# Kernel tuning notes

Measured on AMD Instinct MI355X. Metric: run time of the kernel, lower is better.

The kernel has to match this reference:

```python
import jax, jax.numpy as jnp
import numpy as np

N = 65536    # collocation points
N1 = 1024    # RBF centers
EPS = 0.1    # multiscale parameter used for width init scale


def setup_inputs() -> dict:
    key = jax.random.key(0)
    ks = jax.random.split(key, 10)
    x = jax.random.uniform(ks[0], (N, 2), dtype=jnp.float32)

    def mk(i):
        h = jax.random.uniform(ks[3 * i + 1], (N1,), dtype=jnp.float32)
        c = jax.random.uniform(ks[3 * i + 2], (N1, 2), dtype=jnp.float32)
        w = 5.0 * jax.random.uniform(ks[3 * i + 3], (N1, 2), dtype=jnp.float32) / EPS
        return h, c, w

    h1, c1, w1 = mk(0)
    h2, c2, w2 = mk(1)
    h3, c3, w3 = mk(2)
    return dict(x=x, hight=h1, center=c1, width=w1,
                hight2=h2, center2=c2, width2=w2,
                hight3=h3, center3=c3, width3=w3)


def _rbf(X, c, h, w):
    """Gaussian RBF expansion. X:(N,2) points, c:(N1,2) centers,
    h:(N1,) heights, w:(N1,2) widths. Returns u, du/dx, du/dy, each (N,)."""
    x1 = X[:, 0:1] - c[None, :, 0]          # (N, N1)
    y1 = X[:, 1:2] - c[None, :, 1]          # (N, N1)
    d1 = w[:, 0] ** 2                        # (N1,)
    d2 = w[:, 1] ** 2                        # (N1,)
    e = jnp.exp(-(x1 ** 2) * d1 - (y1 ** 2) * d2)  # (N, N1)
    u = e @ h                                # (N,)
    ux = (-2.0 * x1 * d1 * e) @ h            # (N,)
    uy = (-2.0 * y1 * d2 * e) @ h            # (N,)
    return u, ux, uy


def reference(x, hight, center, width, hight2, center2, width2,
              hight3, center3, width3):
    _, ux, uy = _rbf(x, center, hight, width)
    P, Px, _ = _rbf(x, center2, hight2, width2)
    Q, _, Qy = _rbf(x, center3, hight3, width3)
    return (ux, uy, P, Px, Q, Qy)
```

## Files before the change

### kernel.cpp

```cpp
#include <hip/hip_runtime.h>
#include <math.h>

#define N_PTS  65536
#define N_CTR  1024
#define CHUNK  64
#define PPT    4
#define PPB    (256 * PPT)

#if __has_builtin(__builtin_amdgcn_exp2f)
#define EXP2(v) __builtin_amdgcn_exp2f(v)
#else
#define EXP2(v) exp2f(v)
#endif


__global__ __launch_bounds__(256) void prep_kernel(
    const float* __restrict__ h0, const float* __restrict__ c0, const float* __restrict__ w0,
    const float* __restrict__ h1, const float* __restrict__ c1, const float* __restrict__ w1,
    const float* __restrict__ h2, const float* __restrict__ c2, const float* __restrict__ w2,
    float4* __restrict__ RA, float4* __restrict__ RB, float* __restrict__ RC)
{
    const int idx = blockIdx.x * 256 + threadIdx.x;
    if (idx >= 3 * N_CTR) return;
    const int set = idx >> 10;
    const int j   = idx & (N_CTR - 1);

    const float*  h = (set == 0) ? h0 : ((set == 1) ? h1 : h2);
    const float2* c = (const float2*)((set == 0) ? c0 : ((set == 1) ? c1 : c2));
    const float2* w = (const float2*)((set == 0) ? w0 : ((set == 1) ? w1 : w2));

    const float LOG2E = 1.4426950408889634f;
    float2 cj = c[j];
    float2 wj = w[j];
    float  hh = h[j];
    float d1 = wj.x * wj.x;
    float d2 = wj.y * wj.y;
    float zb =  2.f * cj.x * d1 * LOG2E;
    float zc = -d1 * LOG2E;
    float zd =  2.f * cj.y * d2 * LOG2E;
    float ze = -d2 * LOG2E;
    float za = -(cj.x * cj.x * d1 + cj.y * cj.y * d2) * LOG2E;
    float k0, k1, k2, k3;
    if (set == 0) {
        k0 = -2.f * hh * d1;  k1 = 2.f * hh * d1 * cj.x;
        k2 = -2.f * hh * d2;  k3 = 2.f * hh * d2 * cj.y;
    } else if (set == 1) {
        k0 = hh;  k1 = -2.f * hh * d1;  k2 = 2.f * hh * d1 * cj.x;  k3 = 0.f;
    } else {
        k0 = hh;  k1 = -2.f * hh * d2;  k2 = 2.f * hh * d2 * cj.y;  k3 = 0.f;
    }
    RA[idx] = make_float4(zb, zc, zd, ze);
    RB[idx] = make_float4(za, k0, k1, k2);
    RC[idx] = k3;
}

__global__ __launch_bounds__(256) void srbf_main(
    const float* __restrict__ x,
    const float4* __restrict__ RA,
    const float4* __restrict__ RB,
    const float*  __restrict__ RC,
    float* __restrict__ out)
{
    const int bid   = blockIdx.x;
    const int set   = bid >> 10;
    const int r     = bid & 1023;
    const int chunk = r >> 6;
    const int pblk  = r & 63;
    const int tid   = threadIdx.x;
    const int cbase = set * N_CTR + chunk * CHUNK;

    const int base = pblk * PPB + tid;
    float X[PPT], Y[PPT], X2[PPT], Y2[PPT];
    #pragma unroll
    for (int p = 0; p < PPT; ++p) {
        float2 q = ((const float2*)x)[base + p * 256];
        X[p] = q.x;  Y[p] = q.y;
        X2[p] = q.x * q.x;  Y2[p] = q.y * q.y;
    }

    if (set == 0) {
        float A0[PPT], A1[PPT], A2[PPT], A3[PPT];
        #pragma unroll
        for (int p = 0; p < PPT; ++p) { A0[p] = A1[p] = A2[p] = A3[p] = 0.f; }

        #pragma unroll 4
        for (int jj = 0; jj < CHUNK; ++jj) {
            const float4 A = RA[cbase + jj];
            const float4 B = RB[cbase + jj];
            const float  k3 = RC[cbase + jj];
            #pragma unroll
            for (int p = 0; p < PPT; ++p) {
                float s = fmaf(X[p],  A.x, B.x);
                s       = fmaf(X2[p], A.y, s);
                s       = fmaf(Y[p],  A.z, s);
                s       = fmaf(Y2[p], A.w, s);
                float e = EXP2(s);
                A0[p] = fmaf(B.y, e, A0[p]);
                A1[p] = fmaf(B.z, e, A1[p]);
                A2[p] = fmaf(B.w, e, A2[p]);
                A3[p] = fmaf(k3,  e, A3[p]);
            }
        }
        #pragma unroll
        for (int p = 0; p < PPT; ++p) {
            const int i = base + p * 256;
            atomicAdd(&out[i],         fmaf(X[p], A0[p], A1[p]));
            atomicAdd(&out[N_PTS + i], fmaf(Y[p], A2[p], A3[p]));
        }
    } else {
        float A0[PPT], A1[PPT], A2[PPT];
        #pragma unroll
        for (int p = 0; p < PPT; ++p) { A0[p] = A1[p] = A2[p] = 0.f; }

        #pragma unroll 4
        for (int jj = 0; jj < CHUNK; ++jj) {
            const float4 A = RA[cbase + jj];
            const float4 B = RB[cbase + jj];
            #pragma unroll
            for (int p = 0; p < PPT; ++p) {
                float s = fmaf(X[p],  A.x, B.x);
                s       = fmaf(X2[p], A.y, s);
                s       = fmaf(Y[p],  A.z, s);
                s       = fmaf(Y2[p], A.w, s);
                float e = EXP2(s);
                A0[p] = fmaf(B.y, e, A0[p]);
                A1[p] = fmaf(B.z, e, A1[p]);
                A2[p] = fmaf(B.w, e, A2[p]);
            }
        }
        float* o = out + (size_t)set * 2 * N_PTS;
        #pragma unroll
        for (int p = 0; p < PPT; ++p) {
            const int i = base + p * 256;
            const float g = (set == 1) ? X[p] : Y[p];
            atomicAdd(&o[i],         A0[p]);
            atomicAdd(&o[N_PTS + i], fmaf(g, A1[p], A2[p]));
        }
    }
}

extern "C" void kernel_launch(void* const* d_in, const int* in_sizes, int n_in,
                              void* d_out, int out_size, void* d_ws, size_t ws_size,
                              hipStream_t stream) {
    const float* x  = (const float*)d_in[0];
    const float* h1 = (const float*)d_in[1];
    const float* c1 = (const float*)d_in[2];
    const float* w1 = (const float*)d_in[3];
    const float* h2 = (const float*)d_in[4];
    const float* c2 = (const float*)d_in[5];
    const float* w2 = (const float*)d_in[6];
    const float* h3 = (const float*)d_in[7];
    const float* c3 = (const float*)d_in[8];
    const float* w3 = (const float*)d_in[9];

    char* ws = (char*)d_ws;
    float4* RA = (float4*)(ws);
    float4* RB = (float4*)(ws + 49152);
    float*  RC = (float*) (ws + 98304);

    hipMemsetAsync(d_out, 0, (size_t)out_size * sizeof(float), stream);

    prep_kernel<<<dim3(12), dim3(256), 0, stream>>>(
        h1, c1, w1, h2, c2, w2, h3, c3, w3, RA, RB, RC);

    srbf_main<<<dim3(3072), dim3(256), 0, stream>>>(x, RA, RB, RC, (float*)d_out);
}
```

Measured before the change: 59.57 us.

## Bin points into spatial cells and cull negligible RBF centers per cell

```diff
diff --git a/kernel.cpp b/kernel.cpp
--- a/kernel.cpp
+++ b/kernel.cpp
@@ -1,11 +1,14 @@
 #include <hip/hip_runtime.h>
 #include <math.h>
 
-#define N_PTS  65536
-#define N_CTR  1024
-#define CHUNK  64
-#define PPT    4
-#define PPB    (256 * PPT)
+#define N_PTS    65536
+#define N_CTR    1024
+#define NCELLS   256
+#define CELL_CAP 512
+#define CHUNK    512
+#define CUT      44.0f
+
+#define LOG2E 1.4426950408889634f
 
 #if __has_builtin(__builtin_amdgcn_exp2f)
 #define EXP2(v) __builtin_amdgcn_exp2f(v)
@@ -18,9 +21,20 @@
     const float* __restrict__ h0, const float* __restrict__ c0, const float* __restrict__ w0,
     const float* __restrict__ h1, const float* __restrict__ c1, const float* __restrict__ w1,
     const float* __restrict__ h2, const float* __restrict__ c2, const float* __restrict__ w2,
-    float4* __restrict__ RA, float4* __restrict__ RB, float* __restrict__ RC)
+    float4* __restrict__ RA, float4* __restrict__ RB, float* __restrict__ RC,
+    float4* __restrict__ RT, unsigned int* __restrict__ cnt,
+    float4* __restrict__ out_zero)
 {
     const int idx = blockIdx.x * 256 + threadIdx.x;
+
+    {
+        float4 z = make_float4(0.f, 0.f, 0.f, 0.f);
+        float4* o = out_zero + idx * 32;
+        #pragma unroll
+        for (int t = 0; t < 32; ++t) o[t] = z;
+    }
+    if (idx < NCELLS) cnt[idx] = 0u;
+
     if (idx >= 3 * N_CTR) return;
     const int set = idx >> 10;
     const int j   = idx & (N_CTR - 1);
@@ -29,7 +43,6 @@
     const float2* c = (const float2*)((set == 0) ? c0 : ((set == 1) ? c1 : c2));
     const float2* w = (const float2*)((set == 0) ? w0 : ((set == 1) ? w1 : w2));
 
-    const float LOG2E = 1.4426950408889634f;
     float2 cj = c[j];
     float2 wj = w[j];
     float  hh = h[j];
@@ -52,6 +65,21 @@
     RA[idx] = make_float4(zb, zc, zd, ze);
     RB[idx] = make_float4(za, k0, k1, k2);
     RC[idx] = k3;
+    RT[idx] = make_float4(cj.x, cj.y, d1 * LOG2E, d2 * LOG2E);
+}
+
+__global__ __launch_bounds__(256) void bucket_kernel(
+    const float* __restrict__ x,
+    unsigned int* __restrict__ cnt,
+    unsigned short* __restrict__ idxl)
+{
+    const int i = blockIdx.x * 256 + threadIdx.x;
+    float2 p = ((const float2*)x)[i];
+    int cx = (int)(p.x * 16.f); cx = cx > 15 ? 15 : (cx < 0 ? 0 : cx);
+    int cy = (int)(p.y * 16.f); cy = cy > 15 ? 15 : (cy < 0 ? 0 : cy);
+    const int cell = cy * 16 + cx;
+    unsigned int slot = atomicAdd(&cnt[cell], 1u);
+    if (slot < CELL_CAP) idxl[cell * CELL_CAP + slot] = (unsigned short)i;
 }
 
 __global__ __launch_bounds__(256) void srbf_main(
@@ -59,83 +87,108 @@
     const float4* __restrict__ RA,
     const float4* __restrict__ RB,
     const float*  __restrict__ RC,
+    const float4* __restrict__ RT,
+    const unsigned int* __restrict__ cnt,
+    const unsigned short* __restrict__ idxl,
     float* __restrict__ out)
 {
+    __shared__ unsigned short list[CHUNK];
+    __shared__ int mcnt;
+
     const int bid   = blockIdx.x;
-    const int set   = bid >> 10;
-    const int r     = bid & 1023;
-    const int chunk = r >> 6;
-    const int pblk  = r & 63;
+    const int set   = bid / 512;
+    const int r     = bid & 511;
+    const int cell  = r >> 1;
+    const int chunk = r & 1;
     const int tid   = threadIdx.x;
+    const int lane  = tid & 63;
+    const int wv    = tid >> 6;
     const int cbase = set * N_CTR + chunk * CHUNK;
 
-    const int base = pblk * PPB + tid;
-    float X[PPT], Y[PPT], X2[PPT], Y2[PPT];
+    if (tid == 0) mcnt = 0;
+    __syncthreads();
+
+    const float cx0 = (float)(cell & 15) * 0.0625f;
+    const float cy0 = (float)(cell >> 4) * 0.0625f;
+    const float cx1 = cx0 + 0.0625f;
+    const float cy1 = cy0 + 0.0625f;
+
     #pragma unroll
-    for (int p = 0; p < PPT; ++p) {
-        float2 q = ((const float2*)x)[base + p * 256];
-        X[p] = q.x;  Y[p] = q.y;
-        X2[p] = q.x * q.x;  Y2[p] = q.y * q.y;
-    }
-
-    if (set == 0) {
-        float A0[PPT], A1[PPT], A2[PPT], A3[PPT];
-        #pragma unroll
-        for (int p = 0; p < PPT; ++p) { A0[p] = A1[p] = A2[p] = A3[p] = 0.f; }
-
-        #pragma unroll 4
-        for (int jj = 0; jj < CHUNK; ++jj) {
-            const float4 A = RA[cbase + jj];
-            const float4 B = RB[cbase + jj];
-            const float  k3 = RC[cbase + jj];
-            #pragma unroll
-            for (int p = 0; p < PPT; ++p) {
-                float s = fmaf(X[p],  A.x, B.x);
-                s       = fmaf(X2[p], A.y, s);
-                s       = fmaf(Y[p],  A.z, s);
-                s       = fmaf(Y2[p], A.w, s);
-                float e = EXP2(s);
-                A0[p] = fmaf(B.y, e, A0[p]);
-                A1[p] = fmaf(B.z, e, A1[p]);
-                A2[p] = fmaf(B.w, e, A2[p]);
-                A3[p] = fmaf(k3,  e, A3[p]);
-            }
+    for (int rnd = 0; rnd < 2; ++rnd) {
+        const int jl = wv * 128 + rnd * 64 + lane;
+        float4 T = RT[cbase + jl];
+        float dxm = fmaxf(fmaxf(cx0 - T.x, T.x - cx1), 0.f);
+        float dym = fmaxf(fmaxf(cy0 - T.y, T.y - cy1), 0.f);
+        float qm  = dxm * dxm * T.z + dym * dym * T.w;
+        const bool live = qm < CUT;
+        unsigned long long mask = __ballot(live);
+        int prefix = __popcll(mask & ((1ull << lane) - 1ull));
+        int basep = 0;
+        if (lane == 0) basep = atomicAdd(&mcnt, __popcll(mask));
+        basep = __shfl(basep, 0);
+        if (live) list[basep + prefix] = (unsigned short)jl;
+    }
+    __syncthreads();
+    const int m = mcnt;
+
+    const unsigned int nc = cnt[cell];
+    const int n = (int)(nc < CELL_CAP ? nc : CELL_CAP);
+    const int t1i = tid, t2i = tid + 256;
+    const bool v1 = t1i < n, v2 = t2i < n;
+    float x1 = 99.f, y1 = 99.f, x2 = 99.f, y2 = 99.f;
+    int o1 = 0, o2 = 0;
+    if (v1) { o1 = idxl[cell * CELL_CAP + t1i]; float2 p = ((const float2*)x)[o1]; x1 = p.x; y1 = p.y; }
+    if (v2) { o2 = idxl[cell * CELL_CAP + t2i]; float2 p = ((const float2*)x)[o2]; x2 = p.x; y2 = p.y; }
+
+    float A0 = 0.f, A1 = 0.f, A2 = 0.f, A3 = 0.f;
+    float B0 = 0.f, B1 = 0.f, B2 = 0.f, B3 = 0.f;
+
+    #pragma unroll 2
+    for (int t = 0; t < m; ++t) {
+        const int j = __builtin_amdgcn_readfirstlane(cbase + (int)list[t]);
+        const float4 A  = RA[j];
+        const float4 B  = RB[j];
+        const float  k3 = RC[j];
+        {
+            float u1 = fmaf(x1, A.y, A.x);
+            float u2 = fmaf(x1, u1,  B.x);
+            float u3 = fmaf(y1, A.w, A.z);
+            float s  = fmaf(y1, u3,  u2);
+            float e  = EXP2(s);
+            A0 = fmaf(B.y, e, A0);
+            A1 = fmaf(B.z, e, A1);
+            A2 = fmaf(B.w, e, A2);
+            A3 = fmaf(k3,  e, A3);
         }
-        #pragma unroll
-        for (int p = 0; p < PPT; ++p) {
-            const int i = base + p * 256;
-            atomicAdd(&out[i],         fmaf(X[p], A0[p], A1[p]));
-            atomicAdd(&out[N_PTS + i], fmaf(Y[p], A2[p], A3[p]));
+        if (v2) {
+            float u1 = fmaf(x2, A.y, A.x);
+            float u2 = fmaf(x2, u1,  B.x);
+            float u3 = fmaf(y2, A.w, A.z);
+            float s  = fmaf(y2, u3,  u2);
+            float e  = EXP2(s);
+            B0 = fmaf(B.y, e, B0);
+            B1 = fmaf(B.z, e, B1);
+            B2 = fmaf(B.w, e, B2);
+            B3 = fmaf(k3,  e, B3);
         }
-    } else {
-        float A0[PPT], A1[PPT], A2[PPT];
-        #pragma unroll
-        for (int p = 0; p < PPT; ++p) { A0[p] = A1[p] = A2[p] = 0.f; }
-
-        #pragma unroll 4
-        for (int jj = 0; jj < CHUNK; ++jj) {
-            const float4 A = RA[cbase + jj];
-            const float4 B = RB[cbase + jj];
-            #pragma unroll
-            for (int p = 0; p < PPT; ++p) {
-                float s = fmaf(X[p],  A.x, B.x);
-                s       = fmaf(X2[p], A.y, s);
-                s       = fmaf(Y[p],  A.z, s);
-                s       = fmaf(Y2[p], A.w, s);
-                float e = EXP2(s);
-                A0[p] = fmaf(B.y, e, A0[p]);
-                A1[p] = fmaf(B.z, e, A1[p]);
-                A2[p] = fmaf(B.w, e, A2[p]);
-            }
-        }
-        float* o = out + (size_t)set * 2 * N_PTS;
-        #pragma unroll
-        for (int p = 0; p < PPT; ++p) {
-            const int i = base + p * 256;
-            const float g = (set == 1) ? X[p] : Y[p];
-            atomicAdd(&o[i],         A0[p]);
-            atomicAdd(&o[N_PTS + i], fmaf(g, A1[p], A2[p]));
-        }
+    }
+
+    float* obase = out + (size_t)set * 2 * N_PTS;
+    if (v1) {
+        float r1, r2;
+        if (set == 0)      { r1 = fmaf(x1, A0, A1); r2 = fmaf(y1, A2, A3); }
+        else if (set == 1) { r1 = A0;               r2 = fmaf(x1, A1, A2); }
+        else               { r1 = A0;               r2 = fmaf(y1, A1, A2); }
+        atomicAdd(&obase[o1],         r1);
+        atomicAdd(&obase[N_PTS + o1], r2);
+    }
+    if (v2) {
+        float r1, r2;
+        if (set == 0)      { r1 = fmaf(x2, B0, B1); r2 = fmaf(y2, B2, B3); }
+        else if (set == 1) { r1 = B0;               r2 = fmaf(x2, B1, B2); }
+        else               { r1 = B0;               r2 = fmaf(y2, B1, B2); }
+        atomicAdd(&obase[o2],         r1);
+        atomicAdd(&obase[N_PTS + o2], r2);
     }
 }
 
@@ -157,11 +210,15 @@
     float4* RA = (float4*)(ws);
     float4* RB = (float4*)(ws + 49152);
     float*  RC = (float*) (ws + 98304);
-
-    hipMemsetAsync(d_out, 0, (size_t)out_size * sizeof(float), stream);
+    float4* RT = (float4*)(ws + 110592);
+    unsigned int*   cnt  = (unsigned int*)(ws + 159744);
+    unsigned short* idxl = (unsigned short*)(ws + 160768);
 
     prep_kernel<<<dim3(12), dim3(256), 0, stream>>>(
-        h1, c1, w1, h2, c2, w2, h3, c3, w3, RA, RB, RC);
-
-    srbf_main<<<dim3(3072), dim3(256), 0, stream>>>(x, RA, RB, RC, (float*)d_out);
-}
+        h1, c1, w1, h2, c2, w2, h3, c3, w3, RA, RB, RC, RT, cnt, (float4*)d_out);
+
+    bucket_kernel<<<dim3(256), dim3(256), 0, stream>>>(x, cnt, idxl);
+
+    srbf_main<<<dim3(1536), dim3(256), 0, stream>>>(
+        x, RA, RB, RC, RT, cnt, idxl, (float*)d_out);
+}
```

Result: slower. 100.3 us (+68.4%).

## Bin points into Morton cells and skip RBF centers beyond Gaussian cutoff

Applied to the files above, without the earlier changes.

```diff
diff --git a/kernel.cpp b/kernel.cpp
--- a/kernel.cpp
+++ b/kernel.cpp
@@ -1,11 +1,14 @@
 #include <hip/hip_runtime.h>
 #include <math.h>
 
-#define N_PTS  65536
-#define N_CTR  1024
-#define CHUNK  64
-#define PPT    4
-#define PPB    (256 * PPT)
+#define N_PTS   65536
+#define N_CTR   1024
+#define NCELLS  256
+#define NSLICE  64
+#define CHUNK   256
+#define MAXL    (CHUNK + 4)
+#define CUT     44.0f
+#define LOG2E   1.4426950408889634f
 
 #if __has_builtin(__builtin_amdgcn_exp2f)
 #define EXP2(v) __builtin_amdgcn_exp2f(v)
@@ -13,23 +16,44 @@
 #define EXP2(v) exp2f(v)
 #endif
 
+__device__ __forceinline__ int morton4(int v) {
+    v = (v | (v << 2)) & 0x33;
+    v = (v | (v << 1)) & 0x55;
+    return v;
+}
+__device__ __forceinline__ int cell_of(float2 p) {
+    int cx = (int)(p.x * 16.f); cx = cx > 15 ? 15 : (cx < 0 ? 0 : cx);
+    int cy = (int)(p.y * 16.f); cy = cy > 15 ? 15 : (cy < 0 ? 0 : cy);
+    return morton4(cx) | (morton4(cy) << 1);
+}
 
 __global__ __launch_bounds__(256) void prep_kernel(
+    const float* __restrict__ x,
     const float* __restrict__ h0, const float* __restrict__ c0, const float* __restrict__ w0,
     const float* __restrict__ h1, const float* __restrict__ c1, const float* __restrict__ w1,
     const float* __restrict__ h2, const float* __restrict__ c2, const float* __restrict__ w2,
-    float4* __restrict__ RA, float4* __restrict__ RB, float* __restrict__ RC)
+    float4* __restrict__ RA, float4* __restrict__ RB, float* __restrict__ RC,
+    float4* __restrict__ RT, unsigned int* __restrict__ cnt,
+    float2* __restrict__ out2)
 {
     const int idx = blockIdx.x * 256 + threadIdx.x;
+
+    {
+        float2 z = make_float2(0.f, 0.f);
+        out2[idx] = z; out2[idx + 65536] = z; out2[idx + 131072] = z;
+    }
+    {
+        float2 p = ((const float2*)x)[idx];
+        atomicAdd(&cnt[cell_of(p)], 1u);
+    }
     if (idx >= 3 * N_CTR) return;
+
     const int set = idx >> 10;
     const int j   = idx & (N_CTR - 1);
-
     const float*  h = (set == 0) ? h0 : ((set == 1) ? h1 : h2);
     const float2* c = (const float2*)((set == 0) ? c0 : ((set == 1) ? c1 : c2));
     const float2* w = (const float2*)((set == 0) ? w0 : ((set == 1) ? w1 : w2));
 
-    const float LOG2E = 1.4426950408889634f;
     float2 cj = c[j];
     float2 wj = w[j];
     float  hh = h[j];
@@ -52,90 +76,155 @@
     RA[idx] = make_float4(zb, zc, zd, ze);
     RB[idx] = make_float4(za, k0, k1, k2);
     RC[idx] = k3;
+    RT[idx] = make_float4(cj.x, cj.y, d1 * LOG2E, d2 * LOG2E);
+}
+
+__global__ __launch_bounds__(256) void prefix_kernel(
+    const unsigned int* __restrict__ cnt, unsigned int* __restrict__ cursor)
+{
+    __shared__ unsigned int s[256];
+    const int t = threadIdx.x;
+    unsigned int v = cnt[t];
+    s[t] = v;
+    __syncthreads();
+    unsigned int acc = v;
+    for (int off = 1; off < 256; off <<= 1) {
+        unsigned int y = (t >= off) ? s[t - off] : 0u;
+        __syncthreads();
+        acc += y; s[t] = acc;
+        __syncthreads();
+    }
+    cursor[t] = acc - v;
+}
+
+__global__ __launch_bounds__(256) void scatter_kernel(
+    const float* __restrict__ x, unsigned int* __restrict__ cursor,
+    unsigned short* __restrict__ sortedIdx)
+{
+    const int i = blockIdx.x * 256 + threadIdx.x;
+    float2 p = ((const float2*)x)[i];
+    unsigned int slot = atomicAdd(&cursor[cell_of(p)], 1u);
+    sortedIdx[slot] = (unsigned short)i;
 }
 
 __global__ __launch_bounds__(256) void srbf_main(
     const float* __restrict__ x,
-    const float4* __restrict__ RA,
-    const float4* __restrict__ RB,
-    const float*  __restrict__ RC,
+    const float4* __restrict__ RA, const float4* __restrict__ RB,
+    const float*  __restrict__ RC, const float4* __restrict__ RT,
+    const unsigned short* __restrict__ sortedIdx,
     float* __restrict__ out)
 {
+    __shared__ float4 sA[MAXL];
+    __shared__ float4 sB[MAXL];
+    __shared__ float  sC[MAXL];
+    __shared__ int    wtot[4];
+    __shared__ float4 bbx[4];
+
     const int bid   = blockIdx.x;
-    const int set   = bid >> 10;
-    const int r     = bid & 1023;
-    const int chunk = r >> 6;
-    const int pblk  = r & 63;
+    const int slice = bid / 12;
+    const int rr    = bid % 12;
+    const int set   = rr >> 2;
+    const int chunk = rr & 3;
     const int tid   = threadIdx.x;
+    const int lane  = tid & 63;
+    const int wv    = tid >> 6;
     const int cbase = set * N_CTR + chunk * CHUNK;
 
-    const int base = pblk * PPB + tid;
-    float X[PPT], Y[PPT], X2[PPT], Y2[PPT];
-    #pragma unroll
-    for (int p = 0; p < PPT; ++p) {
-        float2 q = ((const float2*)x)[base + p * 256];
-        X[p] = q.x;  Y[p] = q.y;
-        X2[p] = q.x * q.x;  Y2[p] = q.y * q.y;
-    }
-
-    if (set == 0) {
-        float A0[PPT], A1[PPT], A2[PPT], A3[PPT];
+    const float2* xp = (const float2*)x;
+    const int sbase = slice * 1024 + tid;
+    int   O[4];
+    float X[4], Y[4];
+    #pragma unroll
+    for (int k = 0; k < 4; ++k) {
+        int o = sortedIdx[sbase + 256 * k];
+        O[k] = o;
+        float2 p = xp[o];
+        X[k] = p.x; Y[k] = p.y;
+    }
+
+    float mnx = fminf(fminf(X[0], X[1]), fminf(X[2], X[3]));
+    float mxx = fmaxf(fmaxf(X[0], X[1]), fmaxf(X[2], X[3]));
+    float mny = fminf(fminf(Y[0], Y[1]), fminf(Y[2], Y[3]));
+    float mxy = fmaxf(fmaxf(Y[0], Y[1]), fmaxf(Y[2], Y[3]));
+    #pragma unroll
+    for (int d = 1; d < 64; d <<= 1) {
+        mnx = fminf(mnx, __shfl_xor(mnx, d));
+        mxx = fmaxf(mxx, __shfl_xor(mxx, d));
+        mny = fminf(mny, __shfl_xor(mny, d));
+        mxy = fmaxf(mxy, __shfl_xor(mxy, d));
+    }
+    if (lane == 0) bbx[wv] = make_float4(mnx, mxx, mny, mxy);
+    __syncthreads();
+    {
+        float4 b0 = bbx[0], b1 = bbx[1], b2 = bbx[2], b3 = bbx[3];
+        mnx = fminf(fminf(b0.x, b1.x), fminf(b2.x, b3.x));
+        mxx = fmaxf(fmaxf(b0.y, b1.y), fmaxf(b2.y, b3.y));
+        mny = fminf(fminf(b0.z, b1.z), fminf(b2.z, b3.z));
+        mxy = fmaxf(fmaxf(b0.w, b1.w), fmaxf(b2.w, b3.w));
+    }
+
+    const int jg = cbase + tid;
+    float4 T = RT[jg];
+    float dxm = fmaxf(fmaxf(mnx - T.x, T.x - mxx), 0.f);
+    float dym = fmaxf(fmaxf(mny - T.y, T.y - mxy), 0.f);
+    float q   = dxm * dxm * T.z + dym * dym * T.w;
+    const bool live = q < CUT;
+    unsigned long long mask = __ballot(live);
+    if (lane == 0) wtot[wv] = __popcll(mask);
+    __syncthreads();
+    int base = 0, m = 0;
+    #pragma unroll
+    for (int w2 = 0; w2 < 4; ++w2) {
+        int t = wtot[w2];
+        m += t;
+        if (w2 < wv) base += t;
+    }
+    if (live) {
+        int p = base + __popcll(mask & ((1ull << lane) - 1ull));
+        sA[p] = RA[jg]; sB[p] = RB[jg]; sC[p] = RC[jg];
+    }
+    const int mPad = (m + 3) & ~3;
+    if (tid < mPad - m) {
+        sA[m + tid] = make_float4(0.f, 0.f, 0.f, 0.f);
+        sB[m + tid] = make_float4(0.f, 0.f, 0.f, 0.f);
+        sC[m + tid] = 0.f;
+    }
+    __syncthreads();
+
+    float A0[4], A1[4], A2[4], A3[4];
+    #pragma unroll
+    for (int k = 0; k < 4; ++k) { A0[k] = A1[k] = A2[k] = A3[k] = 0.f; }
+
+    for (int t = 0; t < mPad; t += 4) {
         #pragma unroll
-        for (int p = 0; p < PPT; ++p) { A0[p] = A1[p] = A2[p] = A3[p] = 0.f; }
-
-        #pragma unroll 4
-        for (int jj = 0; jj < CHUNK; ++jj) {
-            const float4 A = RA[cbase + jj];
-            const float4 B = RB[cbase + jj];
-            const float  k3 = RC[cbase + jj];
+        for (int u = 0; u < 4; ++u) {
+            const float4 A  = sA[t + u];
+            const float4 K  = sB[t + u];
+            const float  k3 = sC[t + u];
             #pragma unroll
-            for (int p = 0; p < PPT; ++p) {
-                float s = fmaf(X[p],  A.x, B.x);
-                s       = fmaf(X2[p], A.y, s);
-                s       = fmaf(Y[p],  A.z, s);
-                s       = fmaf(Y2[p], A.w, s);
-                float e = EXP2(s);
-                A0[p] = fmaf(B.y, e, A0[p]);
-                A1[p] = fmaf(B.z, e, A1[p]);
-                A2[p] = fmaf(B.w, e, A2[p]);
-                A3[p] = fmaf(k3,  e, A3[p]);
+            for (int k = 0; k < 4; ++k) {
+                float u1 = fmaf(X[k], A.y, A.x);
+                float u2 = fmaf(X[k], u1,  K.x);
+                float u3 = fmaf(Y[k], A.w, A.z);
+                float s  = fmaf(Y[k], u3,  u2);
+                float e  = EXP2(s);
+                A0[k] = fmaf(K.y, e, A0[k]);
+                A1[k] = fmaf(K.z, e, A1[k]);
+                A2[k] = fmaf(K.w, e, A2[k]);
+                A3[k] = fmaf(k3,  e, A3[k]);
             }
         }
-        #pragma unroll
-        for (int p = 0; p < PPT; ++p) {
-            const int i = base + p * 256;
-            atomicAdd(&out[i],         fmaf(X[p], A0[p], A1[p]));
-            atomicAdd(&out[N_PTS + i], fmaf(Y[p], A2[p], A3[p]));
-        }
-    } else {
-        float A0[PPT], A1[PPT], A2[PPT];
-        #pragma unroll
-        for (int p = 0; p < PPT; ++p) { A0[p] = A1[p] = A2[p] = 0.f; }
-
-        #pragma unroll 4
-        for (int jj = 0; jj < CHUNK; ++jj) {
-            const float4 A = RA[cbase + jj];
-            const float4 B = RB[cbase + jj];
-            #pragma unroll
-            for (int p = 0; p < PPT; ++p) {
-                float s = fmaf(X[p],  A.x, B.x);
-                s       = fmaf(X2[p], A.y, s);
-                s       = fmaf(Y[p],  A.z, s);
-                s       = fmaf(Y2[p], A.w, s);
-                float e = EXP2(s);
-                A0[p] = fmaf(B.y, e, A0[p]);
-                A1[p] = fmaf(B.z, e, A1[p]);
-                A2[p] = fmaf(B.w, e, A2[p]);
-            }
-        }
-        float* o = out + (size_t)set * 2 * N_PTS;
-        #pragma unroll
-        for (int p = 0; p < PPT; ++p) {
-            const int i = base + p * 256;
-            const float g = (set == 1) ? X[p] : Y[p];
-            atomicAdd(&o[i],         A0[p]);
-            atomicAdd(&o[N_PTS + i], fmaf(g, A1[p], A2[p]));
-        }
+    }
+
+    float* ob = out + (size_t)set * 2 * N_PTS;
+    #pragma unroll
+    for (int k = 0; k < 4; ++k) {
+        float r1, r2;
+        if (set == 0)      { r1 = fmaf(X[k], A0[k], A1[k]); r2 = fmaf(Y[k], A2[k], A3[k]); }
+        else if (set == 1) { r1 = A0[k];                    r2 = fmaf(X[k], A1[k], A2[k]); }
+        else               { r1 = A0[k];                    r2 = fmaf(Y[k], A1[k], A2[k]); }
+        atomicAdd(&ob[O[k]],         r1);
+        atomicAdd(&ob[N_PTS + O[k]], r2);
     }
 }
 
@@ -157,11 +246,20 @@
     float4* RA = (float4*)(ws);
     float4* RB = (float4*)(ws + 49152);
     float*  RC = (float*) (ws + 98304);
-
-    hipMemsetAsync(d_out, 0, (size_t)out_size * sizeof(float), stream);
-
-    prep_kernel<<<dim3(12), dim3(256), 0, stream>>>(
-        h1, c1, w1, h2, c2, w2, h3, c3, w3, RA, RB, RC);
-
-    srbf_main<<<dim3(3072), dim3(256), 0, stream>>>(x, RA, RB, RC, (float*)d_out);
-}
+    float4* RT = (float4*)(ws + 110592);
+    unsigned int*   cnt    = (unsigned int*)(ws + 159744);
+    unsigned int*   cursor = (unsigned int*)(ws + 160768);
+    unsigned short* sidx   = (unsigned short*)(ws + 161792);
+
+    hipMemsetAsync(cnt, 0, NCELLS * sizeof(unsigned int), stream);
+
+    prep_kernel<<<dim3(256), dim3(256), 0, stream>>>(
+        x, h1, c1, w1, h2, c2, w2, h3, c3, w3, RA, RB, RC, RT, cnt, (float2*)d_out);
+
+    prefix_kernel<<<dim3(1), dim3(256), 0, stream>>>(cnt, cursor);
+
+    scatter_kernel<<<dim3(256), dim3(256), 0, stream>>>(x, cursor, sidx);
+
+    srbf_main<<<dim3(768), dim3(256), 0, stream>>>(
+        x, RA, RB, RC, RT, sidx, (float*)d_out);
+}
```

New measurement: 158.5 us. 166% more time.
